# Performance work log

Hardware: AMD Instinct MI355X
Metric: run time of the kernel (lower is better)

Reference implementation:

```python
import jax, jax.numpy as jnp
import numpy as np

B, T, D, H = 2, 4096, 512, 8
HD = D // H

def setup_inputs() -> dict:
    key = jax.random.key(0)
    ks = jax.random.split(key, 5)
    x = jax.random.normal(ks[0], (B, T, D), dtype=jnp.float32)
    # causal mask: masked_fill where mask == 0
    mask = jnp.tril(jnp.ones((T, T), dtype=jnp.int32))[None, None, :, :]
    qkv_w = jax.random.normal(ks[1], (D, 3 * D), dtype=jnp.float32) * (D ** -0.5)
    qkv_b = jax.random.normal(ks[2], (3 * D,), dtype=jnp.float32) * 0.02
    proj_w = jax.random.normal(ks[3], (D, D), dtype=jnp.float32) * (D ** -0.5)
    proj_b = jax.random.normal(ks[4], (D,), dtype=jnp.float32) * 0.02
    return {"x": x, "mask": mask, "qkv_w": qkv_w, "qkv_b": qkv_b,
            "proj_w": proj_w, "proj_b": proj_b}

def reference(x, mask, qkv_w, qkv_b, proj_w, proj_b):
    b, t, c = x.shape
    qkv = x @ qkv_w + qkv_b                      # [B,T,3D]
    q, k, v = jnp.split(qkv, 3, axis=-1)
    # [B,T,D] -> [B,H,T,hd]
    def heads(a):
        return a.reshape(b, t, H, HD).transpose(0, 2, 1, 3)
    q, k, v = heads(q), heads(k), heads(v)
    att = jnp.einsum('bhqd,bhkd->bhqk', q, k) / (HD ** 0.5)
    att = jnp.where(mask == 0, -jnp.inf, att)
    att = jax.nn.softmax(att, axis=-1)           # dropout p=0.0 -> identity
    out = jnp.einsum('bhqk,bhkd->bhqd', att, v)  # [B,H,T,hd]
    out = out.transpose(0, 2, 1, 3).reshape(b, t, c)
    return out @ proj_w + proj_b
```

## Files before the change

### kernel.cpp

```cpp
#include <hip/hip_runtime.h>
#include <hip/hip_bf16.h>


typedef __attribute__((ext_vector_type(8))) short bf16x8;
typedef __attribute__((ext_vector_type(4))) float f32x4;
typedef __attribute__((ext_vector_type(16))) float f32x16;
typedef __attribute__((ext_vector_type(2))) int i32x2;

#define DEV static __device__ __forceinline__

DEV unsigned short f2bf(float f) {
    union { float f; unsigned u; } a; a.f = f;
    unsigned r = a.u + 0x7FFFu + ((a.u >> 16) & 1u);
    return (unsigned short)(r >> 16);
}

DEV unsigned pack2(float a, float b) {
    unsigned r;
    asm("v_cvt_pk_bf16_f32 %0, %1, %2" : "=v"(r) : "v"(a), "v"(b));
    return r;
}

DEV void glds16(const void* g, void* l) {
    __builtin_amdgcn_global_load_lds(
        (const __attribute__((address_space(1))) void*)g,
        (__attribute__((address_space(3))) void*)l,
        16, 0, 0);
}

DEV f32x4 mfma(bf16x8 a, bf16x8 b, f32x4 c) {
    return __builtin_amdgcn_mfma_f32_16x16x32_bf16(a, b, c, 0, 0, 0);
}

DEV f32x16 mfma32(bf16x8 a, bf16x8 b, f32x16 c) {
    return __builtin_amdgcn_mfma_f32_32x32x16_bf16(a, b, c, 0, 0, 0);
}

DEV void plswap(unsigned& a, unsigned& b) {
#if __has_builtin(__builtin_amdgcn_permlane32_swap)
    i32x2 r = __builtin_amdgcn_permlane32_swap((int)a, (int)b, false, false);
    a = (unsigned)r.x; b = (unsigned)r.y;
#else
    unsigned sa = __shfl_xor(a, 32), sb = __shfl_xor(b, 32);
    bool hi = (threadIdx.x & 32) != 0;
    unsigned na = hi ? sb : a;
    unsigned nb = hi ? b : sa;
    a = na; b = nb;
#endif
}

DEV float xhalf_sum(float x) {
    unsigned a = __float_as_uint(x), b = a;
    plswap(a, b);
    return __uint_as_float(a) + __uint_as_float(b);
}

__global__ __launch_bounds__(256) void k_cast(const float* __restrict__ x,
                                              unsigned short* __restrict__ xb, int n4) {
    for (int i = blockIdx.x * 256 + threadIdx.x; i < n4; i += gridDim.x * 256) {
        float4 v = ((const float4*)x)[i];
        ushort4 o;
        o.x = f2bf(v.x); o.y = f2bf(v.y); o.z = f2bf(v.z); o.w = f2bf(v.w);
        ((ushort4*)xb)[i] = o;
    }
}

__global__ __launch_bounds__(256) void k_tcast2(const float* __restrict__ qkv_w,
                                                unsigned short* __restrict__ wqkvT,
                                                const float* __restrict__ proj_w,
                                                unsigned short* __restrict__ wprojT) {
    __shared__ float t[64][65];
    const int tid = threadIdx.x;
    int id = blockIdx.x;
    const float* src; unsigned short* dst; int R, C, bx, by;
    if (id < 192) { src = qkv_w; dst = wqkvT; R = 512; C = 1536; bx = id % 24; by = id / 24; }
    else { id -= 192; src = proj_w; dst = wprojT; R = 512; C = 512; bx = id & 7; by = id >> 3; }
#pragma unroll
    for (int e = 0; e < 16; ++e) {
        int idx = e * 256 + tid;
        int r = idx >> 6, c = idx & 63;
        t[r][c] = src[(by * 64 + r) * C + bx * 64 + c];
    }
    __syncthreads();
#pragma unroll
    for (int e = 0; e < 16; ++e) {
        int idx = e * 256 + tid;
        int r = idx >> 6, c = idx & 63;
        dst[(bx * 64 + r) * R + by * 64 + c] = f2bf(t[c][r]);
    }
}

__global__ __launch_bounds__(256) void k_gemm_qkv(
    const unsigned short* __restrict__ xb, const unsigned short* __restrict__ wT,
    const float* __restrict__ bias,
    unsigned short* __restrict__ Qb, unsigned short* __restrict__ Kb,
    unsigned short* __restrict__ Vtb)
{
    __shared__ __attribute__((aligned(16))) unsigned short lA[128 * 64];
    __shared__ __attribute__((aligned(16))) unsigned short lB[128 * 64];
    const int tid = threadIdx.x, lane = tid & 63, w = tid >> 6;
    const int qi = lane & 15, g = lane >> 4;
    const int bm = blockIdx.x & 63, bn = blockIdx.x >> 6;
    const int m0 = bm * 128, n0 = bn * 128;
    const int wr = w >> 1, wc = w & 1;
    const int srow = lane >> 3, sch = (lane & 7) ^ srow;
    const int swz = (qi & 7) << 4;
    f32x4 zero = {0.f, 0.f, 0.f, 0.f};
    f32x4 acc[4][4];
#pragma unroll
    for (int i = 0; i < 4; ++i)
#pragma unroll
        for (int j = 0; j < 4; ++j) acc[i][j] = zero;

    for (int kt = 0; kt < 8; ++kt) {
#pragma unroll
        for (int i = 0; i < 4; ++i) {
            int c = w * 4 + i;
            int row = c * 8 + srow;
            glds16(xb + (m0 + row) * 512 + kt * 64 + sch * 8, (char*)lA + c * 1024);
            glds16(wT + (n0 + row) * 512 + kt * 64 + sch * 8, (char*)lB + c * 1024);
        }
        __syncthreads();
#pragma unroll
        for (int k2 = 0; k2 < 2; ++k2) {
            bf16x8 af[4], bfr[4];
#pragma unroll
            for (int i = 0; i < 4; ++i) {
                int ra = wr * 64 + i * 16 + qi;
                af[i] = *(const bf16x8*)((const char*)lA + ra * 128 + ((k2 * 64 + g * 16) ^ swz));
                int rb = wc * 64 + i * 16 + qi;
                bfr[i] = *(const bf16x8*)((const char*)lB + rb * 128 + ((k2 * 64 + g * 16) ^ swz));
            }
#pragma unroll
            for (int mi = 0; mi < 4; ++mi)
#pragma unroll
                for (int ni = 0; ni < 4; ++ni)
                    acc[mi][ni] = mfma(af[mi], bfr[ni], acc[mi][ni]);
        }
        __syncthreads();
    }

    const int comp = n0 >> 9;
#pragma unroll
    for (int mi = 0; mi < 4; ++mi) {
        int mbase = m0 + wr * 64 + mi * 16 + g * 4;
        int b = mbase >> 12, t = mbase & 4095;
#pragma unroll
        for (int ni = 0; ni < 4; ++ni) {
            int n = n0 + wc * 64 + ni * 16 + qi;
            float bn = bias[n];
            int nn = n & 511;
            int h = nn >> 6, d = nn & 63;
            if (comp == 0) {
                unsigned short* dst = Qb + ((b * 8 + h) * 4096 + t) * 64 + d;
#pragma unroll
                for (int r = 0; r < 4; ++r)
                    dst[r * 64] = f2bf((acc[mi][ni][r] + bn) * 0.18033688011112042f);
            } else if (comp == 1) {
                unsigned short* dst = Kb + ((b * 8 + h) * 4096 + t) * 64 + d;
#pragma unroll
                for (int r = 0; r < 4; ++r)
                    dst[r * 64] = f2bf(acc[mi][ni][r] + bn);
            } else {
                ushort4 pk4;
                pk4.x = f2bf(acc[mi][ni][0] + bn);
                pk4.y = f2bf(acc[mi][ni][1] + bn);
                pk4.z = f2bf(acc[mi][ni][2] + bn);
                pk4.w = f2bf(acc[mi][ni][3] + bn);
                *(ushort4*)(Vtb + ((b * 8 + h) * 64 + d) * 4096 + t) = pk4;
            }
        }
    }
}

__global__ __launch_bounds__(512) void k_attn(
    const unsigned short* __restrict__ Qb, const unsigned short* __restrict__ Kb,
    const unsigned short* __restrict__ Vtb, unsigned short* __restrict__ Ob)
{
    __shared__ __attribute__((aligned(16))) char smem[131072];
    const int tid = threadIdx.x, lane = tid & 63, w = tid >> 6;
    const int l31 = lane & 31, l7 = lane & 7, h = lane >> 5;
    const int pr = w >> 1, sub = w & 1;
    const int idx = blockIdx.x;
    const int bh = idx & 15;
    const int p = idx >> 4;
    const unsigned short* Qh = Qb + bh * 4096 * 64;
    const unsigned short* Kh = Kb + bh * 4096 * 64;
    const unsigned short* Vh = Vtb + bh * 4096 * 64;
    const float NEGINF = -__builtin_inff();

    char* base = smem + pr * 32768;
    char* myK0 = base;          char* myV0 = base + 8192;
    char* myK1 = base + 16384;  char* myV1 = base + 24576;

    const int srw = lane >> 3;
    const int sxor = (l7 ^ srw) * 8;
    const int kOffE = (sub * 32 + srw) * 64 + sxor;
    const int vOffE = (sub * 32 + srw) * 4096 + sxor;
    const int ldsO = sub * 4096;

    const int rowbase = l31 * 128;
    int cx[4];
#pragma unroll
    for (int c = 0; c < 4; ++c) cx[c] = ((2 * c + h) ^ l7) * 16;

    const int qrel = (sub << 5) + l31;

    f32x16 z16;
#pragma unroll
    for (int r = 0; r < 16; ++r) z16[r] = 0.f;

    for (int si = 0; si < 2; ++si) {
        const int qt = si ? p : 63 - p;
        const int Tmax = (qt >> 2) + 1;
        const int myT = (qt >= pr) ? ((qt - pr) >> 2) + 1 : 0;
        const int qrow = qt * 64 + sub * 32 + l31;

        bf16x8 qf[4];
#pragma unroll
        for (int c = 0; c < 4; ++c)
            qf[c] = *(const bf16x8*)(Qh + qrow * 64 + 16 * c + 8 * h);

        f32x16 o0 = z16, o1 = z16;
        float li = 0.f;

        if (myT > 0) {
            const unsigned short* kp = Kh + pr * 4096 + kOffE;
            const unsigned short* vp = Vh + vOffE + pr * 64;
#pragma unroll
            for (int i = 0; i < 4; ++i) {
                glds16(kp + i * 512,   myK0 + ldsO + i * 1024);
                glds16(vp + i * 32768, myV0 + ldsO + i * 1024);
            }
        }

        for (int t = 0; t < Tmax; ++t) {
            const int cur = t & 1;
            const bool act  = t < myT;
            const bool actn = (t + 1) < myT;
            if (actn) {
                const int jn = 4 * (t + 1) + pr;
                const unsigned short* kp = Kh + jn * 4096 + kOffE;
                const unsigned short* vp = Vh + vOffE + jn * 64;
                char* kd = cur ? myK0 : myK1;
                char* vd = cur ? myV0 : myV1;
#pragma unroll
                for (int i = 0; i < 4; ++i) {
                    glds16(kp + i * 512,   kd + ldsO + i * 1024);
                    glds16(vp + i * 32768, vd + ldsO + i * 1024);
                }
                asm volatile("s_waitcnt vmcnt(8)" ::: "memory");
            } else {
                asm volatile("s_waitcnt vmcnt(0)" ::: "memory");
            }
            __builtin_amdgcn_s_barrier();
            __builtin_amdgcn_sched_barrier(0);

            if (act) {
                const int j = 4 * t + pr;
                const char* lk = cur ? myK1 : myK0;
                const char* lv = cur ? myV1 : myV0;
                f32x16 s0, s1;
                __builtin_amdgcn_s_setprio(1);
                {
                    bf16x8 k0 = *(const bf16x8*)(lk + rowbase + cx[0]);
                    bf16x8 k1 = *(const bf16x8*)(lk + 4096 + rowbase + cx[0]);
                    s0 = mfma32(k0, qf[0], z16);
                    s1 = mfma32(k1, qf[0], z16);
                }
#pragma unroll
                for (int c = 1; c < 4; ++c) {
                    bf16x8 k0 = *(const bf16x8*)(lk + rowbase + cx[c]);
                    bf16x8 k1 = *(const bf16x8*)(lk + 4096 + rowbase + cx[c]);
                    s0 = mfma32(k0, qf[c], s0);
                    s1 = mfma32(k1, qf[c], s1);
                }
                __builtin_amdgcn_s_setprio(0);

                if (j == qt) {
#pragma unroll
                    for (int r = 0; r < 16; ++r) {
                        int rr = 4 * h + (r & 3) + 8 * (r >> 2);
                        if (rr > qrel) s0[r] = NEGINF;
                        if (rr + 32 > qrel) s1[r] = NEGINF;
                    }
                }

#pragma unroll
                for (int r = 0; r < 16; ++r) {
                    s0[r] = __builtin_amdgcn_exp2f(s0[r]);
                    s1[r] = __builtin_amdgcn_exp2f(s1[r]);
                }
                float a8[8];
#pragma unroll
                for (int r = 0; r < 8; ++r)
                    a8[r] = (s0[r] + s0[r + 8]) + (s1[r] + s1[r + 8]);
                float b0 = (a8[0] + a8[4]) + (a8[1] + a8[5]);
                float b1 = (a8[2] + a8[6]) + (a8[3] + a8[7]);
                li += xhalf_sum(b0 + b1);

                __builtin_amdgcn_s_setprio(1);
#pragma unroll
                for (int c2 = 0; c2 < 4; ++c2) {
                    unsigned u0w, u1w, u2w, u3w;
                    if (c2 < 2) {
                        const int b0i = 8 * c2;
                        u0w = pack2(s0[b0i + 0], s0[b0i + 1]);
                        u1w = pack2(s0[b0i + 2], s0[b0i + 3]);
                        u2w = pack2(s0[b0i + 4], s0[b0i + 5]);
                        u3w = pack2(s0[b0i + 6], s0[b0i + 7]);
                    } else {
                        const int b0i = 8 * (c2 - 2);
                        u0w = pack2(s1[b0i + 0], s1[b0i + 1]);
                        u1w = pack2(s1[b0i + 2], s1[b0i + 3]);
                        u2w = pack2(s1[b0i + 4], s1[b0i + 5]);
                        u3w = pack2(s1[b0i + 6], s1[b0i + 7]);
                    }
                    plswap(u0w, u2w);
                    plswap(u1w, u3w);
                    union { unsigned u[4]; bf16x8 v; } pf;
                    pf.u[0] = u0w; pf.u[1] = u1w; pf.u[2] = u2w; pf.u[3] = u3w;
                    bf16x8 v0 = *(const bf16x8*)(lv + rowbase + cx[c2]);
                    bf16x8 v1 = *(const bf16x8*)(lv + 4096 + rowbase + cx[c2]);
                    o0 = mfma32(v0, pf.v, o0);
                    o1 = mfma32(v1, pf.v, o1);
                }
                __builtin_amdgcn_s_setprio(0);
            }
            __builtin_amdgcn_s_barrier();
            __builtin_amdgcn_sched_barrier(0);
        }

        float* fsm = (float*)smem;
        if (pr != 0) {
            float* slot = fsm + ((((pr - 1) << 1) + sub) * 64 + lane) * 36;
#pragma unroll
            for (int r4 = 0; r4 < 4; ++r4) {
                f32x4 v0 = {o0[4 * r4], o0[4 * r4 + 1], o0[4 * r4 + 2], o0[4 * r4 + 3]};
                f32x4 v1 = {o1[4 * r4], o1[4 * r4 + 1], o1[4 * r4 + 2], o1[4 * r4 + 3]};
                *(f32x4*)(slot + 4 * r4) = v0;
                *(f32x4*)(slot + 16 + 4 * r4) = v1;
            }
            slot[32] = li;
        }
        __syncthreads();
        if (pr == 0) {
            float l = li;
#pragma unroll
            for (int i = 0; i < 3; ++i) {
                const float* s = fsm + (((i << 1) + sub) * 64 + lane) * 36;
                l += s[32];
#pragma unroll
                for (int r4 = 0; r4 < 4; ++r4) {
                    f32x4 a = *(const f32x4*)(s + 4 * r4);
                    f32x4 b = *(const f32x4*)(s + 16 + 4 * r4);
#pragma unroll
                    for (int e = 0; e < 4; ++e) {
                        o0[4 * r4 + e] += a[e];
                        o1[4 * r4 + e] += b[e];
                    }
                }
            }
            float inv = 1.f / l;
            unsigned short* orow = Ob + ((bh >> 3) * 4096 + qrow) * 512 + (bh & 7) * 64 + 4 * h;
#pragma unroll
            for (int g2 = 0; g2 < 4; ++g2) {
                union { ushort4 s4; unsigned u[2]; } a;
                a.u[0] = pack2(o0[4 * g2 + 0] * inv, o0[4 * g2 + 1] * inv);
                a.u[1] = pack2(o0[4 * g2 + 2] * inv, o0[4 * g2 + 3] * inv);
                *(ushort4*)(orow + 8 * g2) = a.s4;
                a.u[0] = pack2(o1[4 * g2 + 0] * inv, o1[4 * g2 + 1] * inv);
                a.u[1] = pack2(o1[4 * g2 + 2] * inv, o1[4 * g2 + 3] * inv);
                *(ushort4*)(orow + 32 + 8 * g2) = a.s4;
            }
        }
        __syncthreads();
    }
}

__global__ __launch_bounds__(256) void k_gemm_proj(
    const unsigned short* __restrict__ Ob, const unsigned short* __restrict__ wT,
    const float* __restrict__ bias, float* __restrict__ out)
{
    __shared__ __attribute__((aligned(16))) unsigned short lA[128 * 64];
    __shared__ __attribute__((aligned(16))) unsigned short lB[128 * 64];
    const int tid = threadIdx.x, lane = tid & 63, w = tid >> 6;
    const int qi = lane & 15, g = lane >> 4;
    const int bm = blockIdx.x & 63, bn = blockIdx.x >> 6;
    const int m0 = bm * 128, n0 = bn * 128;
    const int wr = w >> 1, wc = w & 1;
    const int srow = lane >> 3, sch = (lane & 7) ^ srow;
    const int swz = (qi & 7) << 4;
    f32x4 zero = {0.f, 0.f, 0.f, 0.f};
    f32x4 acc[4][4];
#pragma unroll
    for (int i = 0; i < 4; ++i)
#pragma unroll
        for (int j = 0; j < 4; ++j) acc[i][j] = zero;

    for (int kt = 0; kt < 8; ++kt) {
#pragma unroll
        for (int i = 0; i < 4; ++i) {
            int c = w * 4 + i;
            int row = c * 8 + srow;
            glds16(Ob + (m0 + row) * 512 + kt * 64 + sch * 8, (char*)lA + c * 1024);
            glds16(wT + (n0 + row) * 512 + kt * 64 + sch * 8, (char*)lB + c * 1024);
        }
        __syncthreads();
#pragma unroll
        for (int k2 = 0; k2 < 2; ++k2) {
            bf16x8 af[4], bfr[4];
#pragma unroll
            for (int i = 0; i < 4; ++i) {
                int ra = wr * 64 + i * 16 + qi;
                af[i] = *(const bf16x8*)((const char*)lA + ra * 128 + ((k2 * 64 + g * 16) ^ swz));
                int rb = wc * 64 + i * 16 + qi;
                bfr[i] = *(const bf16x8*)((const char*)lB + rb * 128 + ((k2 * 64 + g * 16) ^ swz));
            }
#pragma unroll
            for (int mi = 0; mi < 4; ++mi)
#pragma unroll
                for (int ni = 0; ni < 4; ++ni)
                    acc[mi][ni] = mfma(af[mi], bfr[ni], acc[mi][ni]);
        }
        __syncthreads();
    }

#pragma unroll
    for (int mi = 0; mi < 4; ++mi) {
        int mbase = m0 + wr * 64 + mi * 16 + g * 4;
#pragma unroll
        for (int ni = 0; ni < 4; ++ni) {
            int n = n0 + wc * 64 + ni * 16 + qi;
            float bn = bias[n];
#pragma unroll
            for (int r = 0; r < 4; ++r)
                out[(mbase + r) * 512 + n] = acc[mi][ni][r] + bn;
        }
    }
}

extern "C" void kernel_launch(void* const* d_in, const int* in_sizes, int n_in,
                              void* d_out, int out_size, void* d_ws, size_t ws_size,
                              hipStream_t stream) {
    const float* x      = (const float*)d_in[0];
    const float* qkv_w  = (const float*)d_in[2];
    const float* qkv_b  = (const float*)d_in[3];
    const float* proj_w = (const float*)d_in[4];
    const float* proj_b = (const float*)d_in[5];

    char* ws = (char*)d_ws;
    unsigned short* xb     = (unsigned short*)(ws);
    unsigned short* wqkvT  = (unsigned short*)(ws +  8388608);
    unsigned short* wprojT = (unsigned short*)(ws +  9961472);
    unsigned short* Qb     = (unsigned short*)(ws + 10485760);
    unsigned short* Kb     = (unsigned short*)(ws + 18874368);
    unsigned short* Vtb    = (unsigned short*)(ws + 27262976);
    unsigned short* Ob     = (unsigned short*)(ws + 35651584);
    float* out = (float*)d_out;

    k_cast<<<2048, 256, 0, stream>>>(x, xb, 8192 * 512 / 4);
    k_tcast2<<<256, 256, 0, stream>>>(qkv_w, wqkvT, proj_w, wprojT);
    k_gemm_qkv<<<768, 256, 0, stream>>>(xb, wqkvT, qkv_b, Qb, Kb, Vtb);
    k_attn<<<512, 512, 0, stream>>>(Qb, Kb, Vtb, Ob);
    k_gemm_proj<<<256, 256, 0, stream>>>(Ob, wprojT, proj_b, out);
}
```

Before: 114.3 us.

## Replace LDS double buffering with register-staged prefetch and a single LDS buffer

Replaces the double-buffered direct global-to-LDS loads with a register-staged pipeline: the next K/V tile is loaded into registers while the current tile is consumed, then written into a single LDS buffer at the start of each iteration. This halves shared memory use (128KB to 64KB), which could allow more blocks per CU and lower LDS pressure. The cost is extra VGPRs for staging, explicit ds_write instructions, and a full vmcnt(0) wait plus barriers every iteration, which may expose global load latency.

```diff
diff --git a/kernel.cpp b/kernel.cpp
--- a/kernel.cpp
+++ b/kernel.cpp
@@ -177,7 +177,7 @@
     const unsigned short* __restrict__ Qb, const unsigned short* __restrict__ Kb,
     const unsigned short* __restrict__ Vtb, unsigned short* __restrict__ Ob)
 {
-    __shared__ __attribute__((aligned(16))) char smem[131072];
+    __shared__ __attribute__((aligned(16))) char smem[65536];
     const int tid = threadIdx.x, lane = tid & 63, w = tid >> 6;
     const int l31 = lane & 31, l7 = lane & 7, h = lane >> 5;
     const int pr = w >> 1, sub = w & 1;
@@ -189,15 +189,14 @@
     const unsigned short* Vh = Vtb + bh * 4096 * 64;
     const float NEGINF = -__builtin_inff();
 
-    char* base = smem + pr * 32768;
-    char* myK0 = base;          char* myV0 = base + 8192;
-    char* myK1 = base + 16384;  char* myV1 = base + 24576;
+    char* myK = smem + pr * 16384;
+    char* myV = myK + 8192;
 
     const int srw = lane >> 3;
     const int sxor = (l7 ^ srw) * 8;
     const int kOffE = (sub * 32 + srw) * 64 + sxor;
     const int vOffE = (sub * 32 + srw) * 4096 + sxor;
-    const int ldsO = sub * 4096;
+    const int ldsO = sub * 4096 + lane * 16;
 
     const int rowbase = l31 * 128;
     int cx[4];
@@ -224,42 +223,50 @@
         f32x16 o0 = z16, o1 = z16;
         float li = 0.f;
 
+        bf16x8 kreg[4], vreg[4];
         if (myT > 0) {
             const unsigned short* kp = Kh + pr * 4096 + kOffE;
             const unsigned short* vp = Vh + vOffE + pr * 64;
 #pragma unroll
             for (int i = 0; i < 4; ++i) {
-                glds16(kp + i * 512,   myK0 + ldsO + i * 1024);
-                glds16(vp + i * 32768, myV0 + ldsO + i * 1024);
+                kreg[i] = *(const bf16x8*)(kp + i * 512);
+                vreg[i] = *(const bf16x8*)(vp + i * 32768);
             }
         }
 
         for (int t = 0; t < Tmax; ++t) {
-            const int cur = t & 1;
             const bool act  = t < myT;
             const bool actn = (t + 1) < myT;
+
+            asm volatile("s_waitcnt vmcnt(0)" ::: "memory");
+            __builtin_amdgcn_s_barrier();
+            __builtin_amdgcn_sched_barrier(0);
+
+            if (act) {
+#pragma unroll
+                for (int i = 0; i < 4; ++i) {
+                    *(bf16x8*)(myK + ldsO + i * 1024) = kreg[i];
+                    *(bf16x8*)(myV + ldsO + i * 1024) = vreg[i];
+                }
+            }
             if (actn) {
                 const int jn = 4 * (t + 1) + pr;
                 const unsigned short* kp = Kh + jn * 4096 + kOffE;
                 const unsigned short* vp = Vh + vOffE + jn * 64;
-                char* kd = cur ? myK0 : myK1;
-                char* vd = cur ? myV0 : myV1;
 #pragma unroll
                 for (int i = 0; i < 4; ++i) {
-                    glds16(kp + i * 512,   kd + ldsO + i * 1024);
-                    glds16(vp + i * 32768, vd + ldsO + i * 1024);
-                }
-                asm volatile("s_waitcnt vmcnt(8)" ::: "memory");
-            } else {
-                asm volatile("s_waitcnt vmcnt(0)" ::: "memory");
-            }
+                    kreg[i] = *(const bf16x8*)(kp + i * 512);
+                    vreg[i] = *(const bf16x8*)(vp + i * 32768);
+                }
+            }
+            asm volatile("s_waitcnt lgkmcnt(0)" ::: "memory");
             __builtin_amdgcn_s_barrier();
             __builtin_amdgcn_sched_barrier(0);
 
             if (act) {
                 const int j = 4 * t + pr;
-                const char* lk = cur ? myK1 : myK0;
-                const char* lv = cur ? myV1 : myV0;
+                const char* lk = myK;
+                const char* lv = myV;
                 f32x16 s0, s1;
                 __builtin_amdgcn_s_setprio(1);
                 {
@@ -327,11 +334,10 @@
                 }
                 __builtin_amdgcn_s_setprio(0);
             }
-            __builtin_amdgcn_s_barrier();
-            __builtin_amdgcn_sched_barrier(0);
         }
 
         float* fsm = (float*)smem;
+        __syncthreads();
         if (pr != 0) {
             float* slot = fsm + ((((pr - 1) << 1) + sub) * 64 + lane) * 36;
 #pragma unroll
```

New measurement: 115.7 us. No clear change (+1.3%).
